# Optimization experiments

Measured on AMD Instinct MI355X. Metric: run time of the kernel, lower is better.

## Reference

```python
import jax, jax.numpy as jnp
import numpy as np

N_NODES = 100000
IN_CH = 128
HID = 16
N_EDGES = 3200000


def setup_inputs() -> dict:
    key = jax.random.key(0)
    k1, k2, k3, k4 = jax.random.split(key, 4)
    x = jax.random.normal(k1, (N_NODES, IN_CH), dtype=jnp.float32)
    edge_index = jax.random.randint(k2, (2, N_EDGES), 0, N_NODES, dtype=jnp.int64)
    s1 = 1.0 / np.sqrt(IN_CH)
    s2 = 1.0 / np.sqrt(HID)
    W1 = jax.random.uniform(k3, (IN_CH, HID), dtype=jnp.float32, minval=-s1, maxval=s1)
    b1 = jnp.zeros((HID,), dtype=jnp.float32)
    W2 = jax.random.uniform(k4, (HID, HID), dtype=jnp.float32, minval=-s2, maxval=s2)
    b2 = jnp.zeros((HID,), dtype=jnp.float32)
    return {"x": x, "edge_index": edge_index, "W1": W1, "b1": b1, "W2": W2, "b2": b2}


def _gcn_layer(h, W, b, row, col, norm, n_nodes):
    # GCNConv: transform first (small hidden dim), then normalized sum aggregation
    h = h @ W  # [N, out]
    msg = h[row] * norm[:, None]  # gather over edges incl. self-loops
    out = jax.ops.segment_sum(msg, col, num_segments=n_nodes)
    return out + b


def reference(x, edge_index, W1, b1, W2, b2):
    n = x.shape[0]
    row, col = edge_index[0], edge_index[1]
    # add self-loops (PyG GCNConv default)
    loop = jnp.arange(n, dtype=edge_index.dtype)
    row_l = jnp.concatenate([row, loop])
    col_l = jnp.concatenate([col, loop])
    # symmetric normalization D^-1/2 (A+I) D^-1/2 (degree from target index)
    deg = jax.ops.segment_sum(jnp.ones_like(col_l, dtype=x.dtype), col_l, num_segments=n)
    dinv = jnp.where(deg > 0, jax.lax.rsqrt(deg), 0.0)
    norm = dinv[row_l] * dinv[col_l]

    h = _gcn_layer(x, W1, b1, row_l, col_l, norm, n)
    h = jax.nn.relu(h)  # dropout is identity at eval
    h = _gcn_layer(h, W2, b2, row_l, col_l, norm, n)

    # fused per-edge dot-product link score + sigmoid (original edges only)
    scores = jnp.sum(h[row] * h[col], axis=-1)
    return jax.nn.sigmoid(scores)
```

## Files before the change

### kernel.cpp

```cpp
#include <hip/hip_runtime.h>
#include <hip/hip_bf16.h>
#include <hip/hip_fp16.h>
#include <math.h>


#define BSH 8
#define BSZ 256
#define PA_BLOCKS 256

__global__ __launch_bounds__(512) void pA(const int* __restrict__ col,
                                          int* __restrict__ M, int E, int CH, int NBUK) {
    extern __shared__ int hist[];
    const int t = threadIdx.x, b = blockIdx.x;
    for (int i = t; i < NBUK; i += 512) hist[i] = 0;
    __syncthreads();
    const int s = b * CH, e = min(E, s + CH);
    for (int i = s + t; i < e; i += 512) atomicAdd(&hist[col[i] >> BSH], 1);
    __syncthreads();
    for (int i = t; i < NBUK; i += 512) M[b * NBUK + i] = hist[i];
}

__global__ __launch_bounds__(256) void pB1(int* __restrict__ M, int* __restrict__ T, int NBUK) {
    __shared__ int s[256];
    const int t = threadIdx.x, k = blockIdx.x;
    int own = M[t * NBUK + k];
    s[t] = own;
    __syncthreads();
    for (int d = 1; d < 256; d <<= 1) {
        int add = (t >= d) ? s[t - d] : 0;
        __syncthreads();
        s[t] += add;
        __syncthreads();
    }
    M[t * NBUK + k] = s[t] - own;
    if (t == 255) T[k] = s[255];
}

__global__ __launch_bounds__(512) void pB2(const int* __restrict__ T, int* __restrict__ S,
                                           int* __restrict__ start, int NBUK, int N, int E) {
    __shared__ int s[512];
    const int t = threadIdx.x;
    int own = (t < NBUK) ? T[t] : 0;
    s[t] = own;
    __syncthreads();
    for (int d = 1; d < 512; d <<= 1) {
        int add = (t >= d) ? s[t - d] : 0;
        __syncthreads();
        s[t] += add;
        __syncthreads();
    }
    if (t < NBUK) S[t] = s[t] - own;
    if (t == 511) S[NBUK] = s[511];
    if (t == 0) start[N] = E;
}

__global__ __launch_bounds__(512) void pC(const int* __restrict__ row, const int* __restrict__ col,
                                          const int* __restrict__ M, const int* __restrict__ S,
                                          unsigned int* __restrict__ ebuf, int E, int CH, int NBUK) {
    extern __shared__ int cur[];
    const int t = threadIdx.x, b = blockIdx.x;
    for (int i = t; i < NBUK; i += 512) cur[i] = S[i] + M[b * NBUK + i];
    __syncthreads();
    const int s = b * CH, e = min(E, s + CH);
    for (int i = s + t; i < e; i += 512) {
        int c = col[i], r = row[i];
        int p = atomicAdd(&cur[c >> BSH], 1);
        ebuf[p] = ((unsigned int)(c & (BSZ - 1)) << 17) | (unsigned int)r;
    }
}

__global__ __launch_bounds__(256) void pC2(const unsigned int* __restrict__ ebuf,
                                           const int* __restrict__ S,
                                           unsigned int* __restrict__ ebuf2,
                                           float* __restrict__ dinv,
                                           int* __restrict__ start, int N) {
    __shared__ int h[BSZ], sc[BSZ], cur[BSZ];
    const int t = threadIdx.x, k = blockIdx.x;
    h[t] = 0;
    __syncthreads();
    const int s = S[k], e = S[k + 1];
    for (int i = s + t; i < e; i += 256) atomicAdd(&h[ebuf[i] >> 17], 1);
    __syncthreads();
    sc[t] = h[t];
    __syncthreads();
    for (int d = 1; d < 256; d <<= 1) {
        int add = (t >= d) ? sc[t - d] : 0;
        __syncthreads();
        sc[t] += add;
        __syncthreads();
    }
    cur[t] = sc[t] - h[t];
    const int v = (k << BSH) + t;
    if (v < N) {
        dinv[v] = rsqrtf((float)h[t] + 1.0f);
        start[v] = s + cur[t];
    }
    __syncthreads();
    for (int i = s + t; i < e; i += 256) {
        unsigned int w = ebuf[i];
        int p = atomicAdd(&cur[w >> 17], 1);
        ebuf2[s + p] = w;
    }
}

__global__ __launch_bounds__(256) void k_gemm1(
    const float* __restrict__ x, const float* __restrict__ W1,
    const float* __restrict__ dinv, __half* __restrict__ ts, int N) {
    __shared__ float wsT[16 * 132];
    const int tid = threadIdx.x;
    for (int idx = tid; idx < 2048; idx += 256) {
        int k = idx >> 4, c = idx & 15;
        wsT[c * 132 + k] = W1[idx];
    }
    __syncthreads();
    const int n = blockIdx.x * 256 + tid;
    if (n >= N) return;
    const float4* xr = (const float4*)(x + (size_t)n * 128);
    float acc[16];
    #pragma unroll
    for (int c = 0; c < 16; ++c) acc[c] = 0.f;
    #pragma unroll 4
    for (int k4 = 0; k4 < 32; ++k4) {
        float4 a = xr[k4];
        #pragma unroll
        for (int c = 0; c < 16; ++c) {
            const float4 w = *(const float4*)&wsT[c * 132 + k4 * 4];
            acc[c] = fmaf(a.x, w.x, fmaf(a.y, w.y, fmaf(a.z, w.z, fmaf(a.w, w.w, acc[c]))));
        }
    }
    float dv = dinv[n];
    union { __half h[16]; uint4 u[2]; } o;
    #pragma unroll
    for (int c = 0; c < 16; ++c) o.h[c] = __float2half(acc[c] * dv);
    uint4* dst = (uint4*)(ts + (size_t)n * 16);
    dst[0] = o.u[0]; dst[1] = o.u[1];
}

__global__ __launch_bounds__(256) void pGat1(
    const unsigned int* __restrict__ ebuf2, const int* __restrict__ start,
    const __half2* __restrict__ tsv, const float* __restrict__ dinv,
    const float* __restrict__ b1, const float* __restrict__ W2,
    __half2* __restrict__ ts2v, int N) {
    __shared__ float w2s[256];
    const int tid = threadIdx.x;
    w2s[tid] = W2[tid];
    __syncthreads();
    const int l = tid & 7;
    const int v = blockIdx.x * 32 + (tid >> 3);
    if (v >= N) return;
    const int s = start[v], e = start[v + 1];
    float sx = 0.f, sy = 0.f;
    int i = s;
    for (; i + 4 <= e; i += 4) {
        int r0 = ebuf2[i]     & 0x1FFFF;
        int r1 = ebuf2[i + 1] & 0x1FFFF;
        int r2 = ebuf2[i + 2] & 0x1FFFF;
        int r3 = ebuf2[i + 3] & 0x1FFFF;
        float2 f0 = __half22float2(tsv[(size_t)r0 * 8 + l]);
        float2 f1 = __half22float2(tsv[(size_t)r1 * 8 + l]);
        float2 f2 = __half22float2(tsv[(size_t)r2 * 8 + l]);
        float2 f3 = __half22float2(tsv[(size_t)r3 * 8 + l]);
        sx += (f0.x + f1.x) + (f2.x + f3.x);
        sy += (f0.y + f1.y) + (f2.y + f3.y);
    }
    for (; i < e; ++i) {
        int r = ebuf2[i] & 0x1FFFF;
        float2 f = __half22float2(tsv[(size_t)r * 8 + l]);
        sx += f.x; sy += f.y;
    }
    const float dv = dinv[v];
    float2 sf = __half22float2(tsv[(size_t)v * 8 + l]);
    float hx = fmaxf(dv * (sx + sf.x) + b1[2 * l],     0.f);
    float hy = fmaxf(dv * (sy + sf.y) + b1[2 * l + 1], 0.f);
    float ox = 0.f, oy = 0.f;
    #pragma unroll
    for (int j = 0; j < 8; ++j) {
        float ax = __shfl(hx, j, 8);
        float ay = __shfl(hy, j, 8);
        ox = fmaf(ax, w2s[(2 * j) * 16 + 2 * l],     fmaf(ay, w2s[(2 * j + 1) * 16 + 2 * l],     ox));
        oy = fmaf(ax, w2s[(2 * j) * 16 + 2 * l + 1], fmaf(ay, w2s[(2 * j + 1) * 16 + 2 * l + 1], oy));
    }
    ts2v[(size_t)v * 8 + l] = __halves2half2(__float2half(dv * ox), __float2half(dv * oy));
}

__global__ __launch_bounds__(256) void pGat2(
    const unsigned int* __restrict__ ebuf2, const int* __restrict__ start,
    const __half2* __restrict__ tsv, const float* __restrict__ dinv,
    const float* __restrict__ b2, __half2* __restrict__ h2v, int N) {
    const int tid = threadIdx.x;
    const int l = tid & 7;
    const int v = blockIdx.x * 32 + (tid >> 3);
    if (v >= N) return;
    const int s = start[v], e = start[v + 1];
    float sx = 0.f, sy = 0.f;
    int i = s;
    for (; i + 4 <= e; i += 4) {
        int r0 = ebuf2[i]     & 0x1FFFF;
        int r1 = ebuf2[i + 1] & 0x1FFFF;
        int r2 = ebuf2[i + 2] & 0x1FFFF;
        int r3 = ebuf2[i + 3] & 0x1FFFF;
        float2 f0 = __half22float2(tsv[(size_t)r0 * 8 + l]);
        float2 f1 = __half22float2(tsv[(size_t)r1 * 8 + l]);
        float2 f2 = __half22float2(tsv[(size_t)r2 * 8 + l]);
        float2 f3 = __half22float2(tsv[(size_t)r3 * 8 + l]);
        sx += (f0.x + f1.x) + (f2.x + f3.x);
        sy += (f0.y + f1.y) + (f2.y + f3.y);
    }
    for (; i < e; ++i) {
        int r = ebuf2[i] & 0x1FFFF;
        float2 f = __half22float2(tsv[(size_t)r * 8 + l]);
        sx += f.x; sy += f.y;
    }
    float2 sf = __half22float2(tsv[(size_t)v * 8 + l]);
    const float dv = dinv[v];
    h2v[(size_t)v * 8 + l] = __halves2half2(
        __float2half(dv * (sx + sf.x) + b2[2 * l]),
        __float2half(dv * (sy + sf.y) + b2[2 * l + 1]));
}

__global__ void k_score(const int* __restrict__ row, const int* __restrict__ col,
                        const __half* __restrict__ h2h, float* __restrict__ out, int E) {
    int e = blockIdx.x * 256 + threadIdx.x;
    if (e < E) {
        union { uint4 u[2]; __half2 h[8]; } a, b;
        const uint4* pa = (const uint4*)(h2h + (size_t)row[e] * 16);
        const uint4* pb = (const uint4*)(h2h + (size_t)col[e] * 16);
        a.u[0] = pa[0]; a.u[1] = pa[1];
        b.u[0] = pb[0]; b.u[1] = pb[1];
        float d = 0.f;
        #pragma unroll
        for (int i = 0; i < 8; ++i) {
            float2 fa = __half22float2(a.h[i]);
            float2 fb = __half22float2(b.h[i]);
            d = fmaf(fa.x, fb.x, fmaf(fa.y, fb.y, d));
        }
        out[e] = 1.0f / (1.0f + __expf(-d));
    }
}

__global__ void k_countf(const int* __restrict__ col, float* __restrict__ deg, int E) {
    int e = blockIdx.x * 256 + threadIdx.x;
    if (e < E) atomicAdd(&deg[col[e]], 1.0f);
}
__global__ void k_dinvf(float* __restrict__ dinv, int N) {
    int v = blockIdx.x * 256 + threadIdx.x;
    if (v < N) dinv[v] = rsqrtf(dinv[v] + 1.0f);
}
__global__ __launch_bounds__(256) void k_gemm1f(
    const float* __restrict__ x, const float* __restrict__ W1,
    const float* __restrict__ dinv, float* __restrict__ ts, int N) {
    __shared__ float wsT[16 * 132];
    const int tid = threadIdx.x;
    for (int idx = tid; idx < 2048; idx += 256) {
        int k = idx >> 4, c = idx & 15;
        wsT[c * 132 + k] = W1[idx];
    }
    __syncthreads();
    const int n = blockIdx.x * 256 + tid;
    if (n >= N) return;
    const float4* xr = (const float4*)(x + (size_t)n * 128);
    float acc[16];
    #pragma unroll
    for (int c = 0; c < 16; ++c) acc[c] = 0.f;
    for (int k4 = 0; k4 < 32; ++k4) {
        float4 a = xr[k4];
        #pragma unroll
        for (int c = 0; c < 16; ++c) {
            const float4 w = *(const float4*)&wsT[c * 132 + k4 * 4];
            acc[c] = fmaf(a.x, w.x, fmaf(a.y, w.y, fmaf(a.z, w.z, fmaf(a.w, w.w, acc[c]))));
        }
    }
    float dv = dinv[n];
    float4* o = (float4*)(ts + (size_t)n * 16);
    #pragma unroll
    for (int q = 0; q < 4; ++q)
        o[q] = make_float4(acc[4*q] * dv, acc[4*q+1] * dv, acc[4*q+2] * dv, acc[4*q+3] * dv);
}
__global__ void k_scatter(const int* __restrict__ row, const int* __restrict__ col,
                          const float* __restrict__ ts, float* __restrict__ acc, int E) {
    int g = blockIdx.x * 256 + threadIdx.x;
    int e = g >> 4, c = g & 15;
    if (e < E) atomicAdd(&acc[(size_t)col[e] * 16 + c], ts[(size_t)row[e] * 16 + c]);
}
__global__ void k_finalize(float* __restrict__ acc, const float* __restrict__ ts,
                           const float* __restrict__ dinv, const float* __restrict__ b,
                           int N, int relu) {
    int g = blockIdx.x * 256 + threadIdx.x;
    int v = g >> 4, c = g & 15;
    if (v < N) {
        float h = dinv[v] * (acc[g] + ts[g]) + b[c];
        if (relu) h = fmaxf(h, 0.f);
        acc[g] = h;
    }
}
__global__ __launch_bounds__(256) void k_gemm2f(
    const float* __restrict__ h1, const float* __restrict__ W2,
    const float* __restrict__ dinv, float* __restrict__ ts2, int N) {
    __shared__ float hs[16 * 17];
    __shared__ float ws2[256];
    const int tid = threadIdx.x;
    const int base = blockIdx.x * 16;
    if (tid < 64) ((float4*)ws2)[tid] = ((const float4*)W2)[tid];
    if (tid >= 64 && tid < 128) {
        int t2 = tid - 64;
        float4 v4 = ((const float4*)(h1 + (size_t)base * 16))[t2];
        float* d = &hs[(t2 >> 2) * 17 + (t2 & 3) * 4];
        d[0] = v4.x; d[1] = v4.y; d[2] = v4.z; d[3] = v4.w;
    }
    __syncthreads();
    const int r = tid >> 4, c = tid & 15;
    float a = 0.f;
    #pragma unroll
    for (int kk = 0; kk < 16; ++kk) a = fmaf(hs[r * 17 + kk], ws2[kk * 16 + c], a);
    ts2[(size_t)(base + r) * 16 + c] = a * dinv[base + r];
}
__global__ void k_scoref(const int* __restrict__ row, const int* __restrict__ col,
                         const float* __restrict__ h2, float* __restrict__ out, int E) {
    int e = blockIdx.x * 256 + threadIdx.x;
    if (e < E) {
        const float4* a = (const float4*)(h2 + (size_t)row[e] * 16);
        const float4* b = (const float4*)(h2 + (size_t)col[e] * 16);
        float d = 0.f;
        #pragma unroll
        for (int i = 0; i < 4; ++i) {
            float4 u = a[i], v = b[i];
            d += u.x * v.x + u.y * v.y + u.z * v.z + u.w * v.w;
        }
        out[e] = 1.0f / (1.0f + __expf(-d));
    }
}

extern "C" void kernel_launch(void* const* d_in, const int* in_sizes, int n_in,
                              void* d_out, int out_size, void* d_ws, size_t ws_size,
                              hipStream_t stream) {
    const float* x  = (const float*)d_in[0];
    const int*   ei = (const int*)d_in[1];
    const float* W1 = (const float*)d_in[2];
    const float* b1 = (const float*)d_in[3];
    const float* W2 = (const float*)d_in[4];
    const float* b2 = (const float*)d_in[5];

    const int N = in_sizes[0] / 128;
    const int E = in_sizes[1] / 2;
    const int* row = ei;
    const int* col = ei + E;
    float* out = (float*)d_out;

    const int NBUK = (N + BSZ - 1) / BSZ;
    const int CH = (E + PA_BLOCKS - 1) / PA_BLOCKS;

    char* ws = (char*)d_ws;
    size_t off = 0;
    auto alloc = [&](size_t bytes) { void* p = ws + off; off += (bytes + 255) & ~(size_t)255; return p; };
    float*  dinv  = (float*)alloc((size_t)N * 4);
    __half* ts1h  = (__half*)alloc((size_t)N * 32);
    __half* ts2h  = (__half*)alloc((size_t)N * 32);
    int*    start = (int*)alloc((size_t)(N + 1) * 4);
    int*    M     = (int*)alloc((size_t)PA_BLOCKS * NBUK * 4);
    int*    T     = (int*)alloc((size_t)NBUK * 4);
    int*    S     = (int*)alloc((size_t)(NBUK + 1) * 4);
    unsigned int* ebuf  = (unsigned int*)alloc((size_t)E * 4);
    unsigned int* ebuf2 = (unsigned int*)alloc((size_t)E * 4);
    const size_t need = off;

    if (N <= 131072 && NBUK <= 512 && ws_size >= need) {
        const size_t ldsA = (size_t)NBUK * 4;
        pA <<<PA_BLOCKS, 512, ldsA, stream>>>(col, M, E, CH, NBUK);
        pB1<<<NBUK, 256, 0, stream>>>(M, T, NBUK);
        pB2<<<1, 512, 0, stream>>>(T, S, start, NBUK, N, E);
        pC <<<PA_BLOCKS, 512, ldsA, stream>>>(row, col, M, S, ebuf, E, CH, NBUK);
        pC2<<<NBUK, 256, 0, stream>>>(ebuf, S, ebuf2, dinv, start, N);
        k_gemm1<<<(N + 255) / 256, 256, 0, stream>>>(x, W1, dinv, ts1h, N);
        pGat1<<<(N + 31) / 32, 256, 0, stream>>>(ebuf2, start, (const __half2*)ts1h, dinv, b1, W2,
                                                 (__half2*)ts2h, N);
        __half* h2h = ts1h;
        pGat2<<<(N + 31) / 32, 256, 0, stream>>>(ebuf2, start, (const __half2*)ts2h, dinv, b2,
                                                 (__half2*)h2h, N);
        k_score<<<(E + 255) / 256, 256, 0, stream>>>(row, col, h2h, out, E);
    } else {
        float* dinvF = (float*)ws;
        float* ts1F  = (float*)(ws + (size_t)N * 4);
        float* ts2F  = (float*)(ws + (size_t)N * 4 + (size_t)N * 64);
        hipMemsetAsync(dinvF, 0, (size_t)N * 4, stream);
        hipMemsetAsync(ts2F, 0, (size_t)N * 64, stream);
        k_countf<<<(E + 255) / 256, 256, 0, stream>>>(col, dinvF, E);
        k_dinvf<<<(N + 255) / 256, 256, 0, stream>>>(dinvF, N);
        k_gemm1f<<<(N + 255) / 256, 256, 0, stream>>>(x, W1, dinvF, ts1F, N);
        k_scatter<<<(E * 16) / 256, 256, 0, stream>>>(row, col, ts1F, ts2F, E);
        k_finalize<<<(N * 16 + 255) / 256, 256, 0, stream>>>(ts2F, ts1F, dinvF, b1, N, 1);
        k_gemm2f<<<N / 16, 256, 0, stream>>>(ts2F, W2, dinvF, ts1F, N);
        hipMemsetAsync(ts2F, 0, (size_t)N * 64, stream);
        k_scatter<<<(E * 16) / 256, 256, 0, stream>>>(row, col, ts1F, ts2F, E);
        k_finalize<<<(N * 16 + 255) / 256, 256, 0, stream>>>(ts2F, ts1F, dinvF, b2, N, 0);
        k_scoref<<<(E + 255) / 256, 256, 0, stream>>>(row, col, ts2F, out, E);
    }
}
```

Before: 283.5 us.

## Stage CSR bucket scatter in LDS with small chunks and larger buckets

The edge bucketing pass now uses about a thousand fixed 3200-edge chunks instead of 256 large ones. Each chunk first sorts its edges into buckets locally in LDS, then writes them to the global edge buffer in runs that are contiguous per bucket, replacing one random global write per edge. Buckets double to 512 nodes, so there are fewer buckets and the per-bucket pass runs with 512 threads. Column and row reads are vectorised as int4. The cost is a larger per-bucket prefix scan (1024 threads), more LDS per block, and more per-block scan overhead.

```diff
diff --git a/kernel.cpp b/kernel.cpp
--- a/kernel.cpp
+++ b/kernel.cpp
@@ -4,36 +4,47 @@
 #include <math.h>
 
 
-#define BSH 8
-#define BSZ 256
-#define PA_BLOCKS 256
-
-__global__ __launch_bounds__(512) void pA(const int* __restrict__ col,
+#define BSH 9
+#define BSZ 512
+#define MAXCH 3200
+#define MAXCHUNKS 1024
+
+__global__ __launch_bounds__(256) void pA(const int* __restrict__ col,
                                           int* __restrict__ M, int E, int CH, int NBUK) {
-    extern __shared__ int hist[];
+    __shared__ int hist[256];
     const int t = threadIdx.x, b = blockIdx.x;
-    for (int i = t; i < NBUK; i += 512) hist[i] = 0;
+    hist[t] = 0;
     __syncthreads();
     const int s = b * CH, e = min(E, s + CH);
-    for (int i = s + t; i < e; i += 512) atomicAdd(&hist[col[i] >> BSH], 1);
-    __syncthreads();
-    for (int i = t; i < NBUK; i += 512) M[b * NBUK + i] = hist[i];
-}
-
-__global__ __launch_bounds__(256) void pB1(int* __restrict__ M, int* __restrict__ T, int NBUK) {
-    __shared__ int s[256];
+    const int n4 = (e - s) >> 2;
+    const int4* c4 = (const int4*)(col + s);
+    for (int i = t; i < n4; i += 256) {
+        int4 c = c4[i];
+        atomicAdd(&hist[c.x >> BSH], 1);
+        atomicAdd(&hist[c.y >> BSH], 1);
+        atomicAdd(&hist[c.z >> BSH], 1);
+        atomicAdd(&hist[c.w >> BSH], 1);
+    }
+    for (int i = s + (n4 << 2) + t; i < e; i += 256) atomicAdd(&hist[col[i] >> BSH], 1);
+    __syncthreads();
+    for (int i = t; i < NBUK; i += 256) M[b * NBUK + i] = hist[i];
+}
+
+__global__ __launch_bounds__(1024) void pB1(int* __restrict__ M, int* __restrict__ T,
+                                            int NBUK, int CN) {
+    __shared__ int s[1024];
     const int t = threadIdx.x, k = blockIdx.x;
-    int own = M[t * NBUK + k];
+    int own = (t < CN) ? M[t * NBUK + k] : 0;
     s[t] = own;
     __syncthreads();
-    for (int d = 1; d < 256; d <<= 1) {
+    for (int d = 1; d < 1024; d <<= 1) {
         int add = (t >= d) ? s[t - d] : 0;
         __syncthreads();
         s[t] += add;
         __syncthreads();
     }
-    M[t * NBUK + k] = s[t] - own;
-    if (t == 255) T[k] = s[255];
+    if (t < CN) M[t * NBUK + k] = s[t] - own;
+    if (t == 1023) T[k] = s[1023];
 }
 
 __global__ __launch_bounds__(512) void pB2(const int* __restrict__ T, int* __restrict__ S,
@@ -54,22 +65,69 @@
     if (t == 0) start[N] = E;
 }
 
-__global__ __launch_bounds__(512) void pC(const int* __restrict__ row, const int* __restrict__ col,
+__global__ __launch_bounds__(256) void pC(const int* __restrict__ row, const int* __restrict__ col,
                                           const int* __restrict__ M, const int* __restrict__ S,
                                           unsigned int* __restrict__ ebuf, int E, int CH, int NBUK) {
-    extern __shared__ int cur[];
+    __shared__ unsigned int se[MAXCH];
+    __shared__ unsigned short pk[MAXCH];
+    __shared__ int lhist[256], lbase[256], lcur[256], gbase[256];
     const int t = threadIdx.x, b = blockIdx.x;
-    for (int i = t; i < NBUK; i += 512) cur[i] = S[i] + M[b * NBUK + i];
+    lhist[t] = 0;
     __syncthreads();
     const int s = b * CH, e = min(E, s + CH);
-    for (int i = s + t; i < e; i += 512) {
-        int c = col[i], r = row[i];
-        int p = atomicAdd(&cur[c >> BSH], 1);
-        ebuf[p] = ((unsigned int)(c & (BSZ - 1)) << 17) | (unsigned int)r;
-    }
-}
-
-__global__ __launch_bounds__(256) void pC2(const unsigned int* __restrict__ ebuf,
+    const int cnt = e - s;
+    const int n4 = cnt >> 2;
+    const int4* c4 = (const int4*)(col + s);
+    const int4* r4 = (const int4*)(row + s);
+    for (int i = t; i < n4; i += 256) {
+        int4 c = c4[i];
+        atomicAdd(&lhist[c.x >> BSH], 1);
+        atomicAdd(&lhist[c.y >> BSH], 1);
+        atomicAdd(&lhist[c.z >> BSH], 1);
+        atomicAdd(&lhist[c.w >> BSH], 1);
+    }
+    for (int i = (n4 << 2) + t; i < cnt; i += 256) atomicAdd(&lhist[col[s + i] >> BSH], 1);
+    __syncthreads();
+    {
+        int own = lhist[t];
+        lcur[t] = own;
+        __syncthreads();
+        for (int d = 1; d < 256; d <<= 1) {
+            int add = (t >= d) ? lcur[t - d] : 0;
+            __syncthreads();
+            lcur[t] += add;
+            __syncthreads();
+        }
+        lbase[t] = lcur[t] - own;
+        if (t < NBUK) gbase[t] = S[t] + M[b * NBUK + t] - lbase[t];
+        lcur[t] = lbase[t];
+    }
+    __syncthreads();
+    for (int i = t; i < n4; i += 256) {
+        int4 c = c4[i];
+        int4 r = r4[i];
+        int k0 = c.x >> BSH, p0 = atomicAdd(&lcur[k0], 1);
+        se[p0] = ((unsigned int)(c.x & (BSZ - 1)) << 17) | (unsigned int)r.x; pk[p0] = (unsigned short)k0;
+        int k1 = c.y >> BSH, p1 = atomicAdd(&lcur[k1], 1);
+        se[p1] = ((unsigned int)(c.y & (BSZ - 1)) << 17) | (unsigned int)r.y; pk[p1] = (unsigned short)k1;
+        int k2 = c.z >> BSH, p2 = atomicAdd(&lcur[k2], 1);
+        se[p2] = ((unsigned int)(c.z & (BSZ - 1)) << 17) | (unsigned int)r.z; pk[p2] = (unsigned short)k2;
+        int k3 = c.w >> BSH, p3 = atomicAdd(&lcur[k3], 1);
+        se[p3] = ((unsigned int)(c.w & (BSZ - 1)) << 17) | (unsigned int)r.w; pk[p3] = (unsigned short)k3;
+    }
+    for (int i = (n4 << 2) + t; i < cnt; i += 256) {
+        int c = col[s + i], r = row[s + i];
+        int k = c >> BSH, p = atomicAdd(&lcur[k], 1);
+        se[p] = ((unsigned int)(c & (BSZ - 1)) << 17) | (unsigned int)r; pk[p] = (unsigned short)k;
+    }
+    __syncthreads();
+    for (int i = t; i < cnt; i += 256) {
+        int k = pk[i];
+        ebuf[gbase[k] + i] = se[i];
+    }
+}
+
+__global__ __launch_bounds__(512) void pC2(const unsigned int* __restrict__ ebuf,
                                            const int* __restrict__ S,
                                            unsigned int* __restrict__ ebuf2,
                                            float* __restrict__ dinv,
@@ -79,11 +137,11 @@
     h[t] = 0;
     __syncthreads();
     const int s = S[k], e = S[k + 1];
-    for (int i = s + t; i < e; i += 256) atomicAdd(&h[ebuf[i] >> 17], 1);
+    for (int i = s + t; i < e; i += 512) atomicAdd(&h[ebuf[i] >> 17], 1);
     __syncthreads();
     sc[t] = h[t];
     __syncthreads();
-    for (int d = 1; d < 256; d <<= 1) {
+    for (int d = 1; d < 512; d <<= 1) {
         int add = (t >= d) ? sc[t - d] : 0;
         __syncthreads();
         sc[t] += add;
@@ -96,7 +154,7 @@
         start[v] = s + cur[t];
     }
     __syncthreads();
-    for (int i = s + t; i < e; i += 256) {
+    for (int i = s + t; i < e; i += 512) {
         unsigned int w = ebuf[i];
         int p = atomicAdd(&cur[w >> 17], 1);
         ebuf2[s + p] = w;
@@ -347,7 +405,8 @@
     float* out = (float*)d_out;
 
     const int NBUK = (N + BSZ - 1) / BSZ;
-    const int CH = (E + PA_BLOCKS - 1) / PA_BLOCKS;
+    const int CN = (E + MAXCH - 1) / MAXCH;
+    const int CH = MAXCH;
 
     char* ws = (char*)d_ws;
     size_t off = 0;
@@ -356,20 +415,19 @@
     __half* ts1h  = (__half*)alloc((size_t)N * 32);
     __half* ts2h  = (__half*)alloc((size_t)N * 32);
     int*    start = (int*)alloc((size_t)(N + 1) * 4);
-    int*    M     = (int*)alloc((size_t)PA_BLOCKS * NBUK * 4);
+    int*    M     = (int*)alloc((size_t)CN * NBUK * 4);
     int*    T     = (int*)alloc((size_t)NBUK * 4);
     int*    S     = (int*)alloc((size_t)(NBUK + 1) * 4);
     unsigned int* ebuf  = (unsigned int*)alloc((size_t)E * 4);
     unsigned int* ebuf2 = (unsigned int*)alloc((size_t)E * 4);
     const size_t need = off;
 
-    if (N <= 131072 && NBUK <= 512 && ws_size >= need) {
-        const size_t ldsA = (size_t)NBUK * 4;
-        pA <<<PA_BLOCKS, 512, ldsA, stream>>>(col, M, E, CH, NBUK);
-        pB1<<<NBUK, 256, 0, stream>>>(M, T, NBUK);
+    if (N <= 131072 && NBUK <= 256 && CN <= MAXCHUNKS && ws_size >= need) {
+        pA <<<CN, 256, 0, stream>>>(col, M, E, CH, NBUK);
+        pB1<<<NBUK, 1024, 0, stream>>>(M, T, NBUK, CN);
         pB2<<<1, 512, 0, stream>>>(T, S, start, NBUK, N, E);
-        pC <<<PA_BLOCKS, 512, ldsA, stream>>>(row, col, M, S, ebuf, E, CH, NBUK);
-        pC2<<<NBUK, 256, 0, stream>>>(ebuf, S, ebuf2, dinv, start, N);
+        pC <<<CN, 256, 0, stream>>>(row, col, M, S, ebuf, E, CH, NBUK);
+        pC2<<<NBUK, 512, 0, stream>>>(ebuf, S, ebuf2, dinv, start, N);
         k_gemm1<<<(N + 255) / 256, 256, 0, stream>>>(x, W1, dinv, ts1h, N);
         pGat1<<<(N + 31) / 32, 256, 0, stream>>>(ebuf2, start, (const __half2*)ts1h, dinv, b1, W2,
                                                  (__half2*)ts2h, N);
```

Result: faster. 265.1 us (-6.5%).
